# Kernel tuning notes

Measured on AMD Instinct MI355X. Metric: run time of the kernel, lower is better.

The kernel has to match this reference:

```python
import jax, jax.numpy as jnp
import numpy as np


def _sobel_kernels(dtype):
    # Faithful to the torch code: each kernel has shape (1,3,3) in (kd,kh,kw),
    # i.e. a 2D Sobel applied slice-wise, but conv3d uses padding=1 on ALL dims
    # so the output depth is D+2.
    sx = np.array([[[-1, 0, 1], [-2, 0, 2], [-1, 0, 1]]], dtype=np.float32)  # (1,3,3)
    sy = np.transpose(sx, (0, 2, 1))                                          # transpose(1,2)
    sz = np.array([[[-1, -2, -1], [0, 0, 0], [1, 2, 1]]], dtype=np.float32)
    k = np.stack([sx, sy, sz])[:, None]  # (3 out, 1 in, 1, 3, 3)
    return jnp.asarray(k, dtype)


def setup_inputs() -> dict:
    key = jax.random.key(0)
    k1, k2 = jax.random.split(key)
    B, C, D, H, W = 2, 4, 96, 160, 160
    pred = jax.random.normal(k1, (B, C, D, H, W), dtype=jnp.float32)
    target = jax.random.randint(k2, (B, D, H, W), 0, C)
    return {"pred": pred, "target": target}


def reference(pred, target):
    B, C, D, H, W = pred.shape
    p = jax.nn.softmax(pred, axis=1)                                   # (B,C,D,H,W)
    t = jax.nn.one_hot(target, C, dtype=pred.dtype)                    # (B,D,H,W,C)
    t = jnp.transpose(t, (0, 4, 1, 2, 3))                              # (B,C,D,H,W)
    k = _sobel_kernels(pred.dtype)

    def sobel(x):
        # fold class into batch; 3 output channels = x/y/z gradients
        x = x.reshape(B * C, 1, D, H, W)
        return jax.lax.conv_general_dilated(
            x, k, window_strides=(1, 1, 1), padding=[(1, 1)] * 3,
            dimension_numbers=("NCDHW", "OIDHW", "NCDHW"))           # (B*C,3,D+2,H+2,W+2)

    diff = sobel(p) - sobel(t)
    # Each torch mse_loss averages over a (B,1,D+2,H+2,W+2) tensor; the 3*C
    # means are summed, then divided by num_classes.
    per_tensor = B * (D + 2) * (H + 2) * (W + 2)
    loss = jnp.sum(diff * diff) / per_tensor / C
    return loss
```

## Files before the change

kernel.cpp:

```cpp
#include <hip/hip_runtime.h>

#define NB 2
#define NC 4
#define ND 96
#define NH 160
#define NW 160

constexpr int TH    = 8;
constexpr int SR    = TH + 2;
constexpr int NBAND = NH / TH;
constexpr int PITCH = NW;
constexpr int NCELL = SR * PITCH;
constexpr int NSLOT = NCELL / 4;
constexpr int NPART = NBAND * NB * ND;
constexpr float SCALE = 1.0f / (2.0f * 98.0f * 162.0f * 162.0f * 4.0f);

__device__ __forceinline__ int cell(int i) {
    return (i & ~3) | ((i + (i >> 2)) & 3);
}

__device__ __forceinline__ float4 qcalc(float p0, float p1, float p2, float p3,
                                        int t, bool valid) {
    float4 v = make_float4(0.f, 0.f, 0.f, 0.f);
    if (valid) {
        const float m  = fmaxf(fmaxf(p0, p1), fmaxf(p2, p3));
        const float e0 = __expf(p0 - m);
        const float e1 = __expf(p1 - m);
        const float e2 = __expf(p2 - m);
        const float e3 = __expf(p3 - m);
        const float inv = 1.0f / (e0 + e1 + e2 + e3);
        v.x = e0 * inv - (t == 0 ? 1.f : 0.f);
        v.y = e1 * inv - (t == 1 ? 1.f : 0.f);
        v.z = e2 * inv - (t == 2 ? 1.f : 0.f);
        v.w = e3 * inv - (t == 3 ? 1.f : 0.f);
    }
    return v;
}

__global__ __launch_bounds__(256) void boundary_loss_kernel(
    const float* __restrict__ pred,
    const int*   __restrict__ target,
    float* __restrict__ part)
{
    __shared__ float4 q4s[NCELL];
    __shared__ float wsum[4];

    const int tid   = threadIdx.x;
    const int slice = blockIdx.y;
    const int b     = slice / ND;
    const int d     = slice - b * ND;
    const int y0    = blockIdx.x * TH;

    const size_t cs4   = (size_t)ND * NH * NW / 4;
    const size_t pbase = ((size_t)b * NC * ND + d) * (size_t)(NH * NW);
    const size_t tbase = ((size_t)b * ND + d) * (size_t)(NH * NW);

    const int  rA   = tid / 40;
    const int  cA   = tid - rA * 40;
    const int  gyA  = y0 - 1 + rA;
    const bool vA   = (gyA >= 0) && (gyA < NH);
    const int  gyAc = min(max(gyA, 0), NH - 1);

    const int  sB   = tid + 256;
    const bool hasB = (sB < NSLOT);
    const int  rB   = sB / 40;
    const int  cB   = sB - rB * 40;
    const int  gyB  = y0 - 1 + rB;
    const bool vB   = hasB && (gyB >= 0) && (gyB < NH);
    const int  gyBc = min(max(gyB, 0), NH - 1);

    const float4* ppA = (const float4*)(pred + pbase + (size_t)gyAc * NW) + cA;
    const float4 a0 = ppA[0];
    const float4 a1 = ppA[cs4];
    const float4 a2 = ppA[2 * cs4];
    const float4 a3 = ppA[3 * cs4];
    const int4   ta = ((const int4*)(target + tbase + (size_t)gyAc * NW))[cA];

    const int cBs  = hasB ? cB : 0;
    const int gyBs = hasB ? gyBc : 0;
    const float4* ppB = (const float4*)(pred + pbase + (size_t)gyBs * NW) + cBs;
    const float4 b0 = ppB[0];
    const float4 b1 = ppB[cs4];
    const float4 b2 = ppB[2 * cs4];
    const float4 b3 = ppB[3 * cs4];
    const int4   tb = ((const int4*)(target + tbase + (size_t)gyBs * NW))[cBs];

    {
        const int fA = rA * PITCH + 4 * cA;
        q4s[cell(fA + 0)] = qcalc(a0.x, a1.x, a2.x, a3.x, ta.x, vA);
        q4s[cell(fA + 1)] = qcalc(a0.y, a1.y, a2.y, a3.y, ta.y, vA);
        q4s[cell(fA + 2)] = qcalc(a0.z, a1.z, a2.z, a3.z, ta.z, vA);
        q4s[cell(fA + 3)] = qcalc(a0.w, a1.w, a2.w, a3.w, ta.w, vA);
    }
    if (hasB) {
        const int fB = rB * PITCH + 4 * cB;
        q4s[cell(fB + 0)] = qcalc(b0.x, b1.x, b2.x, b3.x, tb.x, vB);
        q4s[cell(fB + 1)] = qcalc(b0.y, b1.y, b2.y, b3.y, tb.y, vB);
        q4s[cell(fB + 2)] = qcalc(b0.z, b1.z, b2.z, b3.z, tb.z, vB);
        q4s[cell(fB + 3)] = qcalc(b0.w, b1.w, b2.w, b3.w, tb.w, vB);
    }
    __syncthreads();

    float acc = 0.f;
    if (tid < NW) {
        float smm0 = 0.f, sm0 = 0.f, dmm0 = 0.f, dm0 = 0.f;
        float smm1 = 0.f, sm1 = 0.f, dmm1 = 0.f, dm1 = 0.f;
        float smm2 = 0.f, sm2 = 0.f, dmm2 = 0.f, dm2 = 0.f;
        float smm3 = 0.f, sm3 = 0.f, dmm3 = 0.f, dm3 = 0.f;

#define CLS(L, M, R, smm, sm, dmm, dm)                                    \
        do {                                                              \
            const float sn = (L) + 2.f * (M) + (R);                       \
            const float dn = (R) - (L);                                   \
            if (t >= 2) {                                                 \
                const float gx = (dmm) + 2.f * (dm) + dn;                 \
                const float gy = sn - (smm);                              \
                acc += gx * gx + 2.f * gy * gy;                           \
            }                                                             \
            smm = sm; sm = sn; dmm = dm; dm = dn;                         \
        } while (0)

        #pragma unroll
        for (int t = 0; t < SR; ++t) {
            const int base = t * PITCH + tid;
            const float4 qm = q4s[cell(base)];
            float4 ql = make_float4(0.f, 0.f, 0.f, 0.f);
            float4 qr = make_float4(0.f, 0.f, 0.f, 0.f);
            if (tid > 0)      ql = q4s[cell(base - 1)];
            if (tid < NW - 1) qr = q4s[cell(base + 1)];
            CLS(ql.x, qm.x, qr.x, smm0, sm0, dmm0, dm0);
            CLS(ql.y, qm.y, qr.y, smm1, sm1, dmm1, dm1);
            CLS(ql.z, qm.z, qr.z, smm2, sm2, dmm2, dm2);
            CLS(ql.w, qm.w, qr.w, smm3, sm3, dmm3, dm3);
        }
#undef CLS
    }

    #pragma unroll
    for (int off = 32; off > 0; off >>= 1)
        acc += __shfl_down(acc, off, 64);
    if ((tid & 63) == 0) wsum[tid >> 6] = acc;
    __syncthreads();
    if (tid == 0) {
        part[blockIdx.y * NBAND + blockIdx.x] =
            wsum[0] + wsum[1] + wsum[2] + wsum[3];
    }
}

__global__ __launch_bounds__(256) void reduce_partials_kernel(
    const float* __restrict__ part, float* __restrict__ out)
{
    const int tid = threadIdx.x;
    float s = 0.f;
    #pragma unroll
    for (int i = 0; i < NPART / 256; ++i)
        s += part[tid + i * 256];
    #pragma unroll
    for (int off = 32; off > 0; off >>= 1)
        s += __shfl_down(s, off, 64);
    __shared__ float wsum[4];
    if ((tid & 63) == 0) wsum[tid >> 6] = s;
    __syncthreads();
    if (tid == 0)
        out[0] = (wsum[0] + wsum[1] + wsum[2] + wsum[3]) * SCALE;
}

extern "C" void kernel_launch(void* const* d_in, const int* in_sizes, int n_in,
                              void* d_out, int out_size, void* d_ws, size_t ws_size,
                              hipStream_t stream) {
    const float* pred   = (const float*)d_in[0];
    const int*   target = (const int*)d_in[1];
    float*       out    = (float*)d_out;
    float*       part   = (float*)d_ws;

    dim3 grid(NBAND, NB * ND);
    boundary_loss_kernel<<<grid, 256, 0, stream>>>(pred, target, part);
    reduce_partials_kernel<<<1, 256, 0, stream>>>(part, out);
}
```

Measured before the change: 131.9 us.

## Store softmax-minus-onehot tile as packed fp16 and compute Sobel in half2

The shared-memory tile of per-class softmax-minus-onehot values is now stored as two packed half2 arrays instead of a swizzled float4 array, halving LDS footprint and traffic. The stencil arithmetic runs on packed half2 ops, and the edge columns read a zeroed sentinel cell instead of branching. This cuts LDS bandwidth and ALU work per pixel but gives up fp32 precision in the gradient terms, which could shift the accumulated loss.

```diff
diff --git a/kernel.cpp b/kernel.cpp
--- a/kernel.cpp
+++ b/kernel.cpp
@@ -1,4 +1,5 @@
 #include <hip/hip_runtime.h>
+#include <hip/hip_fp16.h>
 
 #define NB 2
 #define NC 4
@@ -9,19 +10,20 @@
 constexpr int TH    = 8;
 constexpr int SR    = TH + 2;
 constexpr int NBAND = NH / TH;
-constexpr int PITCH = NW;
-constexpr int NCELL = SR * PITCH;
-constexpr int NSLOT = NCELL / 4;
+constexpr int NSLOT = SR * NW / 4;
+constexpr int PCELL = SR * NW;
+constexpr int ZCELL = PCELL;
 constexpr int NPART = NBAND * NB * ND;
 constexpr float SCALE = 1.0f / (2.0f * 98.0f * 162.0f * 162.0f * 4.0f);
 
-__device__ __forceinline__ int cell(int i) {
-    return (i & ~3) | ((i + (i >> 2)) & 3);
+__device__ __forceinline__ __half2 ld_h2(const unsigned int* p, int i) {
+    return __builtin_bit_cast(__half2, p[i]);
 }
 
-__device__ __forceinline__ float4 qcalc(float p0, float p1, float p2, float p3,
-                                        int t, bool valid) {
-    float4 v = make_float4(0.f, 0.f, 0.f, 0.f);
+__device__ __forceinline__ void qcalc(float p0, float p1, float p2, float p3,
+                                      int t, bool valid,
+                                      unsigned int& ha, unsigned int& hb) {
+    float q0 = 0.f, q1 = 0.f, q2 = 0.f, q3 = 0.f;
     if (valid) {
         const float m  = fmaxf(fmaxf(p0, p1), fmaxf(p2, p3));
         const float e0 = __expf(p0 - m);
@@ -29,12 +31,13 @@
         const float e2 = __expf(p2 - m);
         const float e3 = __expf(p3 - m);
         const float inv = 1.0f / (e0 + e1 + e2 + e3);
-        v.x = e0 * inv - (t == 0 ? 1.f : 0.f);
-        v.y = e1 * inv - (t == 1 ? 1.f : 0.f);
-        v.z = e2 * inv - (t == 2 ? 1.f : 0.f);
-        v.w = e3 * inv - (t == 3 ? 1.f : 0.f);
+        q0 = e0 * inv - (t == 0 ? 1.f : 0.f);
+        q1 = e1 * inv - (t == 1 ? 1.f : 0.f);
+        q2 = e2 * inv - (t == 2 ? 1.f : 0.f);
+        q3 = e3 * inv - (t == 3 ? 1.f : 0.f);
     }
-    return v;
+    ha = __builtin_bit_cast(unsigned int, __floats2half2_rn(q0, q1));
+    hb = __builtin_bit_cast(unsigned int, __floats2half2_rn(q2, q3));
 }
 
 __global__ __launch_bounds__(256) void boundary_loss_kernel(
@@ -42,7 +45,8 @@
     const int*   __restrict__ target,
     float* __restrict__ part)
 {
-    __shared__ float4 q4s[NCELL];
+    __shared__ unsigned int pa[PCELL + 4];
+    __shared__ unsigned int pb[PCELL + 4];
     __shared__ float wsum[4];
 
     const int tid   = threadIdx.x;
@@ -86,52 +90,61 @@
     const int4   tb = ((const int4*)(target + tbase + (size_t)gyBs * NW))[cBs];
 
     {
-        const int fA = rA * PITCH + 4 * cA;
-        q4s[cell(fA + 0)] = qcalc(a0.x, a1.x, a2.x, a3.x, ta.x, vA);
-        q4s[cell(fA + 1)] = qcalc(a0.y, a1.y, a2.y, a3.y, ta.y, vA);
-        q4s[cell(fA + 2)] = qcalc(a0.z, a1.z, a2.z, a3.z, ta.z, vA);
-        q4s[cell(fA + 3)] = qcalc(a0.w, a1.w, a2.w, a3.w, ta.w, vA);
+        uint4 wa, wb;
+        qcalc(a0.x, a1.x, a2.x, a3.x, ta.x, vA, wa.x, wb.x);
+        qcalc(a0.y, a1.y, a2.y, a3.y, ta.y, vA, wa.y, wb.y);
+        qcalc(a0.z, a1.z, a2.z, a3.z, ta.z, vA, wa.z, wb.z);
+        qcalc(a0.w, a1.w, a2.w, a3.w, ta.w, vA, wa.w, wb.w);
+        ((uint4*)pa)[rA * 40 + cA] = wa;
+        ((uint4*)pb)[rA * 40 + cA] = wb;
     }
     if (hasB) {
-        const int fB = rB * PITCH + 4 * cB;
-        q4s[cell(fB + 0)] = qcalc(b0.x, b1.x, b2.x, b3.x, tb.x, vB);
-        q4s[cell(fB + 1)] = qcalc(b0.y, b1.y, b2.y, b3.y, tb.y, vB);
-        q4s[cell(fB + 2)] = qcalc(b0.z, b1.z, b2.z, b3.z, tb.z, vB);
-        q4s[cell(fB + 3)] = qcalc(b0.w, b1.w, b2.w, b3.w, tb.w, vB);
+        uint4 wa, wb;
+        qcalc(b0.x, b1.x, b2.x, b3.x, tb.x, vB, wa.x, wb.x);
+        qcalc(b0.y, b1.y, b2.y, b3.y, tb.y, vB, wa.y, wb.y);
+        qcalc(b0.z, b1.z, b2.z, b3.z, tb.z, vB, wa.z, wb.z);
+        qcalc(b0.w, b1.w, b2.w, b3.w, tb.w, vB, wa.w, wb.w);
+        ((uint4*)pa)[rB * 40 + cB] = wa;
+        ((uint4*)pb)[rB * 40 + cB] = wb;
     }
+    if (tid == 0) { pa[ZCELL] = 0u; pb[ZCELL] = 0u; }
     __syncthreads();
 
     float acc = 0.f;
     if (tid < NW) {
-        float smm0 = 0.f, sm0 = 0.f, dmm0 = 0.f, dm0 = 0.f;
-        float smm1 = 0.f, sm1 = 0.f, dmm1 = 0.f, dm1 = 0.f;
-        float smm2 = 0.f, sm2 = 0.f, dmm2 = 0.f, dm2 = 0.f;
-        float smm3 = 0.f, sm3 = 0.f, dmm3 = 0.f, dm3 = 0.f;
+        int am = tid;
+        int al = (tid > 0)      ? tid - 1 : ZCELL;
+        int ar = (tid < NW - 1) ? tid + 1 : ZCELL;
+        const int il = (tid > 0)      ? NW : 0;
+        const int ir = (tid < NW - 1) ? NW : 0;
 
-#define CLS(L, M, R, smm, sm, dmm, dm)                                    \
+        const __half2 two = __floats2half2_rn(2.f, 2.f);
+        const __half2 hz  = __floats2half2_rn(0.f, 0.f);
+        __half2 smmA = hz, smA = hz, dmmA = hz, dmA = hz;
+        __half2 smmB = hz, smB = hz, dmmB = hz, dmB = hz;
+
+#define CLS(P, smm, sm, dmm, dm)                                          \
         do {                                                              \
-            const float sn = (L) + 2.f * (M) + (R);                       \
-            const float dn = (R) - (L);                                   \
+            const __half2 l = ld_h2(P, al);                               \
+            const __half2 m = ld_h2(P, am);                               \
+            const __half2 r = ld_h2(P, ar);                               \
+            const __half2 sn = __hadd2(__hfma2(m, two, l), r);            \
+            const __half2 dn = __hsub2(r, l);                             \
             if (t >= 2) {                                                 \
-                const float gx = (dmm) + 2.f * (dm) + dn;                 \
-                const float gy = sn - (smm);                              \
-                acc += gx * gx + 2.f * gy * gy;                           \
+                const __half2 gx = __hadd2(__hfma2(dm, two, dmm), dn);    \
+                const __half2 gy = __hsub2(sn, smm);                      \
+                const __half2 rs = __hfma2(__hmul2(gy, gy), two,          \
+                                           __hmul2(gx, gx));              \
+                acc += __low2float(rs) + __high2float(rs);                \
             }                                                             \
             smm = sm; sm = sn; dmm = dm; dm = dn;                         \
         } while (0)
 
         #pragma unroll
         for (int t = 0; t < SR; ++t) {
-            const int base = t * PITCH + tid;
-            const float4 qm = q4s[cell(base)];
-            float4 ql = make_float4(0.f, 0.f, 0.f, 0.f);
-            float4 qr = make_float4(0.f, 0.f, 0.f, 0.f);
-            if (tid > 0)      ql = q4s[cell(base - 1)];
-            if (tid < NW - 1) qr = q4s[cell(base + 1)];
-            CLS(ql.x, qm.x, qr.x, smm0, sm0, dmm0, dm0);
-            CLS(ql.y, qm.y, qr.y, smm1, sm1, dmm1, dm1);
-            CLS(ql.z, qm.z, qr.z, smm2, sm2, dmm2, dm2);
-            CLS(ql.w, qm.w, qr.w, smm3, sm3, dmm3, dm3);
+            CLS(pa, smmA, smA, dmmA, dmA);
+            CLS(pb, smmB, smB, dmmB, dmB);
+            am += NW; al += il; ar += ir;
         }
 #undef CLS
     }
```

After: 128.1 us. 1.03x faster.
